# Kernel tuning notes

Measured on AMD Instinct MI355X. Metric: run time of the kernel, lower is better.

## Reference

```python
import jax, jax.numpy as jnp
import numpy as np

B, N, C_IN, C_INTER = 32, 2048, 512, 512


def setup_inputs() -> dict:
    key = jax.random.key(0)
    ks = jax.random.split(key, 10)
    s_in = 1.0 / np.sqrt(C_IN)
    s_int = 1.0 / np.sqrt(C_INTER)
    return {
        "query": jax.random.normal(ks[0], (B, N, C_IN), jnp.float32),
        "key": jax.random.normal(ks[1], (B, N, C_IN), jnp.float32),
        "Wq": jax.random.normal(ks[2], (C_IN, C_INTER), jnp.float32) * s_in,
        "bq": jnp.zeros((C_INTER,), jnp.float32),
        "Wk": jax.random.normal(ks[3], (C_IN, C_INTER), jnp.float32) * s_in,
        "bk": jnp.zeros((C_INTER,), jnp.float32),
        "Wv": jax.random.normal(ks[4], (C_IN, C_INTER), jnp.float32) * s_in,
        "bv": jnp.zeros((C_INTER,), jnp.float32),
        "Wo": jax.random.normal(ks[5], (C_INTER, C_INTER), jnp.float32) * s_int,
        "bo": jnp.zeros((C_INTER,), jnp.float32),
    }


def reference(query, key, Wq, bq, Wk, bk, Wv, bv, Wo, bo):
    value = key  # value defaults to key in original forward
    q = jnp.einsum("bnc,cd->bnd", query, Wq) + bq   # [B,N,D]
    k = jnp.einsum("bnc,cd->bnd", key, Wk) + bk
    v = jnp.einsum("bnc,cd->bnd", value, Wv) + bv
    d = q.shape[-1]
    # non-standard scaling: divide by d (not sqrt(d))
    scores = jnp.einsum("bqd,bkd->bqk", q, k) / d    # [B,N,N]
    attn = jax.nn.softmax(scores, axis=-1)
    n_kv = attn.shape[-1]
    # second non-standard scaling: divide by number of keys
    out = jnp.einsum("bqk,bkd->bqd", attn, v) / n_kv
    return jnp.einsum("bnd,de->bne", out, Wo) + bo
```

## Files before the change

### kernel.cpp

```cpp
#include <hip/hip_runtime.h>
#include <stdint.h>

typedef unsigned short u16;
typedef __attribute__((ext_vector_type(8))) short bf16x8;
typedef __attribute__((ext_vector_type(4))) float f32x4;
typedef __attribute__((ext_vector_type(2))) unsigned int u32x2;
typedef __attribute__((ext_vector_type(4))) unsigned int u32x4;

__device__ __forceinline__ float bf2f(u16 u) {
  union { unsigned int i; float f; } v; v.i = ((unsigned int)u) << 16; return v.f;
}
__device__ __forceinline__ u16 f2bf(float f) {
  union { float f; unsigned int i; } v; v.f = f;
  unsigned int x = v.i;
  return (u16)((x + 0x7fffu + ((x >> 16) & 1u)) >> 16);
}

__device__ __forceinline__ void async16(const void* g, void* l) {
  __builtin_amdgcn_global_load_lds(
      (const __attribute__((address_space(1))) void*)g,
      (__attribute__((address_space(3))) void*)l, 16, 0, 0);
}

__global__ __launch_bounds__(256) void cast_f32_to_bf16(
    const float* __restrict__ x, u16* __restrict__ y, long n) {
  long i = ((long)blockIdx.x * blockDim.x + threadIdx.x) * 8;
  long stride = (long)gridDim.x * blockDim.x * 8;
  for (long j = i; j < n; j += stride) {
    float4 a = ((const float4*)(x + j))[0];
    float4 b = ((const float4*)(x + j))[1];
    u32x4 o;
    o.x = (unsigned)f2bf(a.x) | ((unsigned)f2bf(a.y) << 16);
    o.y = (unsigned)f2bf(a.z) | ((unsigned)f2bf(a.w) << 16);
    o.z = (unsigned)f2bf(b.x) | ((unsigned)f2bf(b.y) << 16);
    o.w = (unsigned)f2bf(b.z) | ((unsigned)f2bf(b.w) << 16);
    __builtin_nontemporal_store(o, (u32x4*)(y + j));
  }
}

__global__ __launch_bounds__(256) void castKT(
    const float* __restrict__ Kin, u16* __restrict__ Kb, u16* __restrict__ KbT) {
  __shared__ u16 tile[32][34];
  int t = threadIdx.x;
  long b = blockIdx.z;
  int n0 = blockIdx.x * 32, c0 = blockIdx.y * 32;
  int nr = t >> 3, c4 = (t & 7) * 4;
  float4 v = *(const float4*)(Kin + (b * 2048 + n0 + nr) * 512 + c0 + c4);
  unsigned q0 = f2bf(v.x), q1 = f2bf(v.y), q2 = f2bf(v.z), q3 = f2bf(v.w);
  u32x2 o1; o1.x = q0 | (q1 << 16); o1.y = q2 | (q3 << 16);
  __builtin_nontemporal_store(o1, (u32x2*)(Kb + (b * 2048 + n0 + nr) * 512 + c0 + c4));
  tile[nr][c4] = (u16)q0; tile[nr][c4 + 1] = (u16)q1;
  tile[nr][c4 + 2] = (u16)q2; tile[nr][c4 + 3] = (u16)q3;
  __syncthreads();
  int cr = t >> 3, n4 = (t & 7) * 4;
  unsigned r0 = tile[n4][cr], r1 = tile[n4 + 1][cr];
  unsigned r2 = tile[n4 + 2][cr], r3 = tile[n4 + 3][cr];
  u32x2 o2; o2.x = r0 | (r1 << 16); o2.y = r2 | (r3 << 16);
  __builtin_nontemporal_store(o2, (u32x2*)(KbT + (b * 512 + c0 + cr) * 2048 + n0 + n4));
}

__global__ __launch_bounds__(256) void smallGT(
    const float* __restrict__ Ai, const float* __restrict__ Bi, u16* __restrict__ C) {
  __shared__ float As[16][65], Bs[16][65];
  int t = threadIdx.x;
  int i0 = blockIdx.y * 16, j0 = blockIdx.x * 16;
  int r = t >> 4, c4 = (t & 15) * 4;
  int ty = t >> 4, tx = t & 15;
  float acc = 0.f;
  for (int d0 = 0; d0 < 512; d0 += 64) {
    float4 a = *(const float4*)(Ai + (i0 + r) * 512 + d0 + c4);
    float4 b = *(const float4*)(Bi + (j0 + r) * 512 + d0 + c4);
    __syncthreads();
    As[r][c4] = a.x; As[r][c4 + 1] = a.y; As[r][c4 + 2] = a.z; As[r][c4 + 3] = a.w;
    Bs[r][c4] = b.x; Bs[r][c4 + 1] = b.y; Bs[r][c4 + 2] = b.z; Bs[r][c4 + 3] = b.w;
    __syncthreads();
#pragma unroll
    for (int d = 0; d < 64; ++d) acc += As[ty][d] * Bs[tx][d];
  }
  C[(i0 + ty) * 512 + j0 + tx] = f2bf(acc);
}

__global__ __launch_bounds__(256) void smallW2T(
    const float* __restrict__ Wv, const float* __restrict__ Wo, u16* __restrict__ C) {
  __shared__ float Vs[16][65];
  __shared__ float Os[64][17];
  int t = threadIdx.x;
  int k0 = blockIdx.x * 16, n0 = blockIdx.y * 16;
  int r = t >> 4, c4 = (t & 15) * 4;
  int dd = t >> 2, nn4 = (t & 3) * 4;
  int ty = t >> 4, tx = t & 15;
  float acc = 0.f;
  for (int d0 = 0; d0 < 512; d0 += 64) {
    float4 a = *(const float4*)(Wv + (k0 + r) * 512 + d0 + c4);
    float4 b = *(const float4*)(Wo + (long)(d0 + dd) * 512 + n0 + nn4);
    __syncthreads();
    Vs[r][c4] = a.x; Vs[r][c4 + 1] = a.y; Vs[r][c4 + 2] = a.z; Vs[r][c4 + 3] = a.w;
    Os[dd][nn4] = b.x; Os[dd][nn4 + 1] = b.y; Os[dd][nn4 + 2] = b.z; Os[dd][nn4 + 3] = b.w;
    __syncthreads();
#pragma unroll
    for (int d = 0; d < 64; ++d) acc += Vs[tx][d] * Os[d][ty];
  }
  C[(n0 + ty) * 512 + k0 + tx] = f2bf(acc);
}

__global__ __launch_bounds__(256) void wveck(
    const float* __restrict__ Wk, const float* __restrict__ bq, float* __restrict__ wv) {
  int c = blockIdx.x, t = threadIdx.x;
  float s = 0.f;
  for (int d = t; d < 512; d += 256) s += Wk[c * 512 + d] * bq[d];
  for (int off = 32; off; off >>= 1) s += __shfl_xor(s, off);
  __shared__ float r4[4];
  if ((t & 63) == 0) r4[t >> 6] = s;
  __syncthreads();
  if (t == 0) wv[c] = (r4[0] + r4[1] + r4[2] + r4[3]) * (1.0f / 512.0f);
}

__global__ __launch_bounds__(256) void cveck(
    const float* __restrict__ Wo, const float* __restrict__ bv,
    const float* __restrict__ bo, float* __restrict__ c2) {
  int e = blockIdx.x * 256 + threadIdx.x;
  float s = 0.f;
  for (int d = 0; d < 512; ++d) s += bv[d] * Wo[d * 512 + e];
  c2[e] = s * (1.0f / 2048.0f) + bo[e];
}

__global__ __launch_bounds__(256) void betak(
    const u16* __restrict__ Kb, const float* __restrict__ wv, float* __restrict__ beta) {
  __shared__ float ws[512];
  int t = threadIdx.x, lane = t & 63, wid = t >> 6;
  ws[t] = wv[t];
  ws[t + 256] = wv[t + 256];
  __syncthreads();
  long row = (long)blockIdx.x * 4 + wid;
  bf16x8 v = *(const bf16x8*)(Kb + row * 512 + lane * 8);
  float s = 0.f;
#pragma unroll
  for (int j = 0; j < 8; ++j) s += bf2f((u16)v[j]) * ws[lane * 8 + j];
  for (int off = 32; off; off >>= 1) s += __shfl_xor(s, off);
  if (lane == 0) beta[row] = s;
}

template <int MODE>
__global__ __launch_bounds__(256, 3) void gemm(
    const u16* __restrict__ A, const u16* __restrict__ B,
    const float* __restrict__ bias, long sBias, void* __restrict__ Cout,
    int N, int K, long sA, long sB, long sC, float scale,
    int mT, int nT, int Z, int nfast) {
  __shared__ __align__(16) char lds[2][24576];
  const int t = threadIdx.x;
  const int lane = t & 63;
  const int w = t >> 6;
  const int wm = w >> 1;
  const int wn = w & 1;

  const int wg = blockIdx.x;
  const int nb = mT * nT;
  long z; int within;
  if (Z > 1 && (Z & 7) == 0) {
    int xcd = wg & 7;
    int sub = wg >> 3;
    z = (long)(sub / nb) * 8 + xcd;
    within = sub % nb;
  } else {
    z = wg / nb;
    within = wg % nb;
  }
  int bx, by;
  if (nfast) { by = within % nT; bx = within / nT; }
  else       { bx = within % mT; by = within / mT; }
  const long m0 = (long)bx * 256;
  const int n0 = by * 128;
  const int nt = K >> 5;

  const int srow = w * 16 + (lane >> 2);
  const int koff = 8 * ((lane & 3) ^ ((lane >> 3) & 3));
  const u16* pa = A + z * sA + (m0 + srow) * (long)K + koff;
  const u16* pb = B + z * sB + ((long)(n0 + srow)) * K + koff;
  const int ldsW = w * 1024;

  const int fr = lane & 15;
  const int kb = (lane >> 4) * 16;
  const int sw = ((fr >> 1) & 3) << 4;
  const int aoff = (wm * 128 + fr) * 64 + (kb ^ sw);
  const int boff = 16384 + (wn * 64 + fr) * 64 + (kb ^ sw);

  f32x4 acc[8][4] = {};

  {
    char* d = lds[0] + ldsW;
#pragma unroll
    for (int c = 0; c < 4; ++c) async16(pa + (long)c * 64 * K, d + c * 4096);
#pragma unroll
    for (int c = 0; c < 2; ++c) async16(pb + (long)c * 64 * K, d + 16384 + c * 4096);
    pa += 32; pb += 32;
  }
  __syncthreads();

  int cur = 0;
  for (int tt = 0; tt < nt; ++tt) {
    if (tt + 1 < nt) {
      char* d = lds[cur ^ 1] + ldsW;
#pragma unroll
      for (int c = 0; c < 4; ++c) async16(pa + (long)c * 64 * K, d + c * 4096);
#pragma unroll
      for (int c = 0; c < 2; ++c) async16(pb + (long)c * 64 * K, d + 16384 + c * 4096);
      pa += 32; pb += 32;
    }
    const char* rb = lds[cur];
    bf16x8 bf[4];
#pragma unroll
    for (int ni = 0; ni < 4; ++ni)
      bf[ni] = *(const bf16x8*)(rb + boff + ni * 1024);
    __builtin_amdgcn_s_setprio(1);
#pragma unroll
    for (int mi = 0; mi < 8; ++mi) {
      bf16x8 af = *(const bf16x8*)(rb + aoff + mi * 1024);
#pragma unroll
      for (int ni = 0; ni < 4; ++ni)
        acc[mi][ni] = __builtin_amdgcn_mfma_f32_16x16x32_bf16(af, bf[ni], acc[mi][ni], 0, 0, 0);
    }
    __builtin_amdgcn_s_setprio(0);
    __syncthreads();
    cur ^= 1;
  }

  const int er = (lane >> 4) * 4;
  const int ec = lane & 15;
  float bvv[4];
#pragma unroll
  for (int ni = 0; ni < 4; ++ni)
    bvv[ni] = bias ? bias[z * sBias + n0 + wn * 64 + ni * 16 + ec] : 0.0f;
  if (MODE == 0) {
    u16* Ep = (u16*)lds;
    u16* Cp = (u16*)Cout + z * sC;
#pragma unroll
    for (int p = 0; p < 2; ++p) {
      __syncthreads();
      if (wm == p) {
#pragma unroll
        for (int mi = 0; mi < 8; ++mi)
#pragma unroll
          for (int ni = 0; ni < 4; ++ni)
#pragma unroll
            for (int i = 0; i < 4; ++i)
              Ep[(mi * 16 + er + i) * 136 + wn * 64 + ni * 16 + ec] =
                  f2bf(acc[mi][ni][i] * scale + bvv[ni]);
      }
      __syncthreads();
#pragma unroll
      for (int s = 0; s < 8; ++s) {
        int idx = s * 256 + t;
        int R = idx >> 4;
        int j = idx & 15;
        u32x4 d = *(const u32x4*)(Ep + R * 136 + j * 8);
        __builtin_nontemporal_store(
            d, (u32x4*)(Cp + (m0 + p * 128 + R) * (long)N + n0 + j * 8));
      }
    }
  } else {
    float* Ep = (float*)lds;
    float* Cp = (float*)Cout + z * sC;
#pragma unroll
    for (int p = 0; p < 4; ++p) {
      __syncthreads();
      if (wm == (p >> 1)) {
#pragma unroll
        for (int mi2 = 0; mi2 < 4; ++mi2) {
          int mi = (p & 1) * 4 + mi2;
#pragma unroll
          for (int ni = 0; ni < 4; ++ni)
#pragma unroll
            for (int i = 0; i < 4; ++i)
              Ep[(mi2 * 16 + er + i) * 132 + wn * 64 + ni * 16 + ec] =
                  acc[mi][ni][i] * scale + bvv[ni];
        }
      }
      __syncthreads();
#pragma unroll
      for (int s = 0; s < 8; ++s) {
        int idx = s * 256 + t;
        int R = idx >> 5;
        int j = idx & 31;
        f32x4 d = *(const f32x4*)(Ep + R * 132 + j * 4);
        __builtin_nontemporal_store(
            d, (f32x4*)(Cp + (m0 + p * 64 + R) * (long)N + n0 + j * 4));
      }
    }
  }
}

__global__ __launch_bounds__(256) void softmax_rows(u16* __restrict__ S, float inv) {
  int t = threadIdx.x;
  int lane = t & 63, wv = t >> 6;
  long row = (long)blockIdx.x * 4 + wv;
  u16* p = S + row * 2048;
  uint4 raw[4];
#pragma unroll
  for (int q = 0; q < 4; ++q) raw[q] = ((const uint4*)p)[lane + 64 * q];
  float v[32];
#pragma unroll
  for (int q = 0; q < 4; ++q) {
    unsigned wd[4] = {raw[q].x, raw[q].y, raw[q].z, raw[q].w};
#pragma unroll
    for (int j = 0; j < 4; ++j) {
      v[q * 8 + 2 * j]     = bf2f((u16)(wd[j] & 0xffffu));
      v[q * 8 + 2 * j + 1] = bf2f((u16)(wd[j] >> 16));
    }
  }
  float mx = v[0];
#pragma unroll
  for (int j = 1; j < 32; ++j) mx = fmaxf(mx, v[j]);
  for (int off = 32; off; off >>= 1) mx = fmaxf(mx, __shfl_xor(mx, off));
  float s = 0.f;
#pragma unroll
  for (int j = 0; j < 32; ++j) { v[j] = __expf(v[j] - mx); s += v[j]; }
  for (int off = 32; off; off >>= 1) s += __shfl_xor(s, off);
  float r = inv / s;
#pragma unroll
  for (int q = 0; q < 4; ++q) {
    unsigned o[4];
#pragma unroll
    for (int j = 0; j < 4; ++j)
      o[j] = (unsigned)f2bf(v[q * 8 + 2 * j] * r) |
             ((unsigned)f2bf(v[q * 8 + 2 * j + 1] * r) << 16);
    ((uint4*)p)[lane + 64 * q] = make_uint4(o[0], o[1], o[2], o[3]);
  }
}

extern "C" void kernel_launch(void* const* d_in, const int* in_sizes, int n_in,
                              void* d_out, int out_size, void* d_ws, size_t ws_size,
                              hipStream_t stream) {
  const float* query = (const float*)d_in[0];
  const float* key_  = (const float*)d_in[1];
  const float* Wq = (const float*)d_in[2];
  const float* bq = (const float*)d_in[3];
  const float* Wk = (const float*)d_in[4];
  const float* bk = (const float*)d_in[5];
  const float* Wv = (const float*)d_in[6];
  const float* bv = (const float*)d_in[7];
  const float* Wo = (const float*)d_in[8];
  const float* bo = (const float*)d_in[9];
  (void)bk;
  float* out = (float*)d_out;

  const long tokE = 65536L * 512;
  const long bstride = 2048L * 512;

  char* ws = (char*)d_ws;
  u16* Qb   = (u16*)(ws);
  u16* Kb   = (u16*)(ws + 67108864L);
  u16* KbT  = (u16*)(ws + 134217728L);
  u16* GT   = (u16*)(ws + 201326592L);
  u16* W2T  = (u16*)(ws + 201850880L);
  float* wv   = (float*)(ws + 202375168L);
  float* c2   = (float*)(ws + 202377216L);
  float* beta = (float*)(ws + 202379264L);
  char* Sbase = ws + 203423744L;
  u16* attn = Qb;

  u16* qb = (u16*)d_out;

  long s_avail = (long)ws_size - 203423744L;
  int g = (int)(s_avail / 8388608L);
  if (g < 1) g = 1;
  if (g > 32) g = 32;
  if (g >= 8) g &= ~7;

  cast_f32_to_bf16<<<16384, 256, 0, stream>>>(query, Qb, tokE);
  castKT<<<dim3(64, 16, 32), 256, 0, stream>>>(key_, Kb, KbT);
  smallGT<<<dim3(32, 32), 256, 0, stream>>>(Wk, Wq, GT);
  smallW2T<<<dim3(32, 32), 256, 0, stream>>>(Wv, Wo, W2T);
  wveck<<<512, 256, 0, stream>>>(Wk, bq, wv);
  cveck<<<2, 256, 0, stream>>>(Wo, bv, bo, c2);
  betak<<<16384, 256, 0, stream>>>(Kb, wv, beta);

  gemm<0><<<256 * 4, 256, 0, stream>>>(Qb, GT, nullptr, 0, qb,
                                       512, 512, 0, 0, 0, 1.0f, 256, 4, 1, 0);

  for (int b0 = 0; b0 < 32; b0 += g) {
    int bc = (32 - b0 < g) ? (32 - b0) : g;
    u16* Sg = (u16*)Sbase;
    gemm<0><<<8 * 16 * bc, 256, 0, stream>>>(
        qb + (long)b0 * bstride, Kb + (long)b0 * bstride,
        beta + (long)b0 * 2048, 2048, Sg, 2048, 512,
        bstride, bstride, 2048L * 2048, 1.0f / 512.0f, 8, 16, bc, 0);
    softmax_rows<<<bc * 512, 256, 0, stream>>>(Sg, 1.0f / 2048.0f);
    gemm<0><<<8 * 4 * bc, 256, 0, stream>>>(
        Sg, KbT + (long)b0 * bstride, nullptr, 0,
        attn + (long)b0 * bstride, 512, 2048,
        2048L * 2048, bstride, bstride, 1.0f, 8, 4, bc, 1);
  }

  gemm<2><<<256 * 4, 256, 0, stream>>>(attn, W2T, c2, 0, out,
                                       512, 512, 0, 0, 0, 1.0f, 256, 4, 1, 0);
}
```

Measured before the change: 716.5 us.

## Fuse softmax exp into score GEMM epilogue and triple-buffer GEMM pipeline

```diff
diff --git a/kernel.cpp b/kernel.cpp
--- a/kernel.cpp
+++ b/kernel.cpp
@@ -21,6 +21,13 @@
       (const __attribute__((address_space(1))) void*)g,
       (__attribute__((address_space(3))) void*)l, 16, 0, 0);
 }
+
+#define VMC6 asm volatile("s_waitcnt vmcnt(6)" ::: "memory")
+#define VMC0 asm volatile("s_waitcnt vmcnt(0)" ::: "memory")
+#define RAWBAR()                        \
+  asm volatile("" ::: "memory");        \
+  __builtin_amdgcn_s_barrier();         \
+  asm volatile("" ::: "memory")
 
 __global__ __launch_bounds__(256) void cast_f32_to_bf16(
     const float* __restrict__ x, u16* __restrict__ y, long n) {
@@ -140,13 +147,26 @@
   if (lane == 0) beta[row] = s;
 }
 
-template <int MODE>
-__global__ __launch_bounds__(256, 3) void gemm(
+__global__ __launch_bounds__(256) void rowred(
+    const float* __restrict__ psum, float* __restrict__ rinv, int nrows) {
+  int r = blockIdx.x * 256 + threadIdx.x;
+  if (r >= nrows) return;
+  const float* p = psum + (long)r * 32;
+  float s = 0.f;
+#pragma unroll
+  for (int j = 0; j < 32; ++j) s += p[j];
+  rinv[r] = 1.0f / s;
+}
+
+template <int MODE, int EXPO>
+__global__ __launch_bounds__(256, 2) void gemm(
     const u16* __restrict__ A, const u16* __restrict__ B,
-    const float* __restrict__ bias, long sBias, void* __restrict__ Cout,
+    const float* __restrict__ bias, long sBias,
+    const float* __restrict__ rsc, float* __restrict__ psum,
+    void* __restrict__ Cout,
     int N, int K, long sA, long sB, long sC, float scale,
     int mT, int nT, int Z, int nfast) {
-  __shared__ __align__(16) char lds[2][24576];
+  __shared__ __align__(16) char lds[3][24576];
   const int t = threadIdx.x;
   const int lane = t & 63;
   const int w = t >> 6;
@@ -186,27 +206,28 @@
 
   f32x4 acc[8][4] = {};
 
-  {
-    char* d = lds[0] + ldsW;
-#pragma unroll
-    for (int c = 0; c < 4; ++c) async16(pa + (long)c * 64 * K, d + c * 4096);
-#pragma unroll
-    for (int c = 0; c < 2; ++c) async16(pb + (long)c * 64 * K, d + 16384 + c * 4096);
-    pa += 32; pb += 32;
-  }
-  __syncthreads();
-
-  int cur = 0;
+#define STAGE(SLOT)                                                        \
+  do {                                                                     \
+    char* d_ = lds[SLOT] + ldsW;                                           \
+    _Pragma("unroll") for (int c = 0; c < 4; ++c)                          \
+        async16(pa + (long)c * 64 * K, d_ + c * 4096);                     \
+    _Pragma("unroll") for (int c = 0; c < 2; ++c)                          \
+        async16(pb + (long)c * 64 * K, d_ + 16384 + c * 4096);             \
+    pa += 32; pb += 32;                                                    \
+  } while (0)
+
+  STAGE(0);
+  STAGE(1);
+
+  int slot = 0, stslot = 2;
   for (int tt = 0; tt < nt; ++tt) {
-    if (tt + 1 < nt) {
-      char* d = lds[cur ^ 1] + ldsW;
-#pragma unroll
-      for (int c = 0; c < 4; ++c) async16(pa + (long)c * 64 * K, d + c * 4096);
-#pragma unroll
-      for (int c = 0; c < 2; ++c) async16(pb + (long)c * 64 * K, d + 16384 + c * 4096);
-      pa += 32; pb += 32;
+    if (tt < nt - 1) { VMC6; } else { VMC0; }
+    RAWBAR();
+    if (tt + 2 < nt) {
+      STAGE(stslot);
+      stslot = (stslot == 2) ? 0 : stslot + 1;
     }
-    const char* rb = lds[cur];
+    const char* rb = lds[slot];
     bf16x8 bf[4];
 #pragma unroll
     for (int ni = 0; ni < 4; ++ni)
@@ -220,9 +241,9 @@
         acc[mi][ni] = __builtin_amdgcn_mfma_f32_16x16x32_bf16(af, bf[ni], acc[mi][ni], 0, 0, 0);
     }
     __builtin_amdgcn_s_setprio(0);
-    __syncthreads();
-    cur ^= 1;
-  }
+    slot = (slot == 2) ? 0 : slot + 1;
+  }
+#undef STAGE
 
   const int er = (lane >> 4) * 4;
   const int ec = lane & 15;
@@ -238,13 +259,30 @@
       __syncthreads();
       if (wm == p) {
 #pragma unroll
-        for (int mi = 0; mi < 8; ++mi)
-#pragma unroll
-          for (int ni = 0; ni < 4; ++ni)
-#pragma unroll
-            for (int i = 0; i < 4; ++i)
-              Ep[(mi * 16 + er + i) * 136 + wn * 64 + ni * 16 + ec] =
-                  f2bf(acc[mi][ni][i] * scale + bvv[ni]);
+        for (int mi = 0; mi < 8; ++mi) {
+#pragma unroll
+          for (int i = 0; i < 4; ++i) {
+            int lrow = mi * 16 + er + i;
+            float rv = 1.0f;
+            if (!EXPO && rsc) rv = rsc[z * 2048 + m0 + wm * 128 + lrow];
+            float rs = 0.f;
+#pragma unroll
+            for (int ni = 0; ni < 4; ++ni) {
+              float val = acc[mi][ni][i] * scale + bvv[ni];
+              if (EXPO) { val = __expf(val); rs += val; }
+              else val *= rv;
+              Ep[lrow * 136 + wn * 64 + ni * 16 + ec] = f2bf(val);
+            }
+            if (EXPO) {
+              rs += __shfl_xor(rs, 1);
+              rs += __shfl_xor(rs, 2);
+              rs += __shfl_xor(rs, 4);
+              rs += __shfl_xor(rs, 8);
+              if (ec == 0)
+                psum[((long)z * 2048 + m0 + wm * 128 + lrow) * 32 + by * 2 + wn] = rs;
+            }
+          }
+        }
       }
       __syncthreads();
 #pragma unroll
@@ -253,8 +291,7 @@
         int R = idx >> 4;
         int j = idx & 15;
         u32x4 d = *(const u32x4*)(Ep + R * 136 + j * 8);
-        __builtin_nontemporal_store(
-            d, (u32x4*)(Cp + (m0 + p * 128 + R) * (long)N + n0 + j * 8));
+        *(u32x4*)(Cp + (m0 + p * 128 + R) * (long)N + n0 + j * 8) = d;
       }
     }
   } else {
@@ -286,44 +323,6 @@
             d, (f32x4*)(Cp + (m0 + p * 64 + R) * (long)N + n0 + j * 4));
       }
     }
-  }
-}
-
-__global__ __launch_bounds__(256) void softmax_rows(u16* __restrict__ S, float inv) {
-  int t = threadIdx.x;
-  int lane = t & 63, wv = t >> 6;
-  long row = (long)blockIdx.x * 4 + wv;
-  u16* p = S + row * 2048;
-  uint4 raw[4];
-#pragma unroll
-  for (int q = 0; q < 4; ++q) raw[q] = ((const uint4*)p)[lane + 64 * q];
-  float v[32];
-#pragma unroll
-  for (int q = 0; q < 4; ++q) {
-    unsigned wd[4] = {raw[q].x, raw[q].y, raw[q].z, raw[q].w};
-#pragma unroll
-    for (int j = 0; j < 4; ++j) {
-      v[q * 8 + 2 * j]     = bf2f((u16)(wd[j] & 0xffffu));
-      v[q * 8 + 2 * j + 1] = bf2f((u16)(wd[j] >> 16));
-    }
-  }
-  float mx = v[0];
-#pragma unroll
-  for (int j = 1; j < 32; ++j) mx = fmaxf(mx, v[j]);
-  for (int off = 32; off; off >>= 1) mx = fmaxf(mx, __shfl_xor(mx, off));
-  float s = 0.f;
-#pragma unroll
-  for (int j = 0; j < 32; ++j) { v[j] = __expf(v[j] - mx); s += v[j]; }
-  for (int off = 32; off; off >>= 1) s += __shfl_xor(s, off);
-  float r = inv / s;
-#pragma unroll
-  for (int q = 0; q < 4; ++q) {
-    unsigned o[4];
-#pragma unroll
-    for (int j = 0; j < 4; ++j)
-      o[j] = (unsigned)f2bf(v[q * 8 + 2 * j] * r) |
-             ((unsigned)f2bf(v[q * 8 + 2 * j + 1] * r) << 16);
-    ((uint4*)p)[lane + 64 * q] = make_uint4(o[0], o[1], o[2], o[3]);
   }
 }
 
@@ -355,10 +354,12 @@
   float* wv   = (float*)(ws + 202375168L);
   float* c2   = (float*)(ws + 202377216L);
   float* beta = (float*)(ws + 202379264L);
+  float* rinv = (float*)(ws + 202641408L);
   char* Sbase = ws + 203423744L;
   u16* attn = Qb;
 
   u16* qb = (u16*)d_out;
+  float* psum = (float*)((char*)d_out + 67108864L);
 
   long s_avail = (long)ws_size - 203423744L;
   int g = (int)(s_avail / 8388608L);
@@ -374,23 +375,24 @@
   cveck<<<2, 256, 0, stream>>>(Wo, bv, bo, c2);
   betak<<<16384, 256, 0, stream>>>(Kb, wv, beta);
 
-  gemm<0><<<256 * 4, 256, 0, stream>>>(Qb, GT, nullptr, 0, qb,
-                                       512, 512, 0, 0, 0, 1.0f, 256, 4, 1, 0);
+  gemm<0, 0><<<256 * 4, 256, 0, stream>>>(Qb, GT, nullptr, 0, nullptr, nullptr,
+                                          qb, 512, 512, 0, 0, 0, 1.0f, 256, 4, 1, 0);
 
   for (int b0 = 0; b0 < 32; b0 += g) {
     int bc = (32 - b0 < g) ? (32 - b0) : g;
     u16* Sg = (u16*)Sbase;
-    gemm<0><<<8 * 16 * bc, 256, 0, stream>>>(
+    gemm<0, 1><<<8 * 16 * bc, 256, 0, stream>>>(
         qb + (long)b0 * bstride, Kb + (long)b0 * bstride,
-        beta + (long)b0 * 2048, 2048, Sg, 2048, 512,
+        beta + (long)b0 * 2048, 2048, nullptr, psum, Sg, 2048, 512,
         bstride, bstride, 2048L * 2048, 1.0f / 512.0f, 8, 16, bc, 0);
-    softmax_rows<<<bc * 512, 256, 0, stream>>>(Sg, 1.0f / 2048.0f);
-    gemm<0><<<8 * 4 * bc, 256, 0, stream>>>(
-        Sg, KbT + (long)b0 * bstride, nullptr, 0,
+    rowred<<<(bc * 2048 + 255) / 256, 256, 0, stream>>>(psum, rinv + b0 * 2048,
+                                                        bc * 2048);
+    gemm<0, 0><<<8 * 4 * bc, 256, 0, stream>>>(
+        Sg, KbT + (long)b0 * bstride, nullptr, 0, rinv + b0 * 2048, nullptr,
         attn + (long)b0 * bstride, 512, 2048,
-        2048L * 2048, bstride, bstride, 1.0f, 8, 4, bc, 1);
-  }
-
-  gemm<2><<<256 * 4, 256, 0, stream>>>(attn, W2T, c2, 0, out,
-                                       512, 512, 0, 0, 0, 1.0f, 256, 4, 1, 0);
-}
+        2048L * 2048, bstride, bstride, 1.0f / 2048.0f, 8, 4, bc, 1);
+  }
+
+  gemm<2, 0><<<256 * 4, 256, 0, stream>>>(attn, W2T, c2, 0, nullptr, nullptr,
+                                          out, 512, 512, 0, 0, 0, 1.0f, 256, 4, 1, 0);
+}
```

Result: slower. 736.5 us (+2.8%).
